# Optimization experiments

Measured on AMD Instinct MI355X. Metric: run time of the kernel, lower is better.

Reference implementation:

```python
import jax, jax.numpy as jnp
import numpy as np

IN_FEATURES = 4096
OUT_FEATURES = 4096
NUM_SUBVECTORS = 32
NUM_CENTROIDS = 256
SUBVECTOR_DIM = IN_FEATURES // NUM_SUBVECTORS
BATCH, SEQ = 4, 2048


def setup_inputs() -> dict:
    key = jax.random.key(0)
    kx, kc, ka = jax.random.split(key, 3)
    x = jax.random.normal(kx, (BATCH, SEQ, IN_FEATURES), dtype=jnp.float32)
    # Stacked per-subvector codebooks: [S, C, d_sub]
    codebooks = jax.random.normal(kc, (NUM_SUBVECTORS, NUM_CENTROIDS, SUBVECTOR_DIM), dtype=jnp.float32)
    assignments = jax.random.randint(ka, (OUT_FEATURES, NUM_SUBVECTORS), 0, NUM_CENTROIDS, dtype=jnp.int32)
    return {"x": x, "codebooks": codebooks, "assignments": assignments}


def reference(x, codebooks, assignments):
    S = codebooks.shape[0]
    # Gather per-subvector centroids: W_parts[o, s, :] = codebooks[s, assignments[o, s], :]
    sub_idx = jnp.arange(S)[None, :]                      # [1, S]
    w_parts = codebooks[sub_idx, assignments]             # [out, S, d_sub]
    W = w_parts.reshape(w_parts.shape[0], -1)             # [out, in] (concat over subvectors)
    return jnp.einsum('bsi,oi->bso', x, W)                # x @ W.T
```

## Files before the change

### kernel.cpp

```cpp
#include <hip/hip_runtime.h>
#include <hip/hip_bf16.h>


#define K_DIM 4096
#define N_DIM 4096
#define M_DIM 8192

typedef __attribute__((ext_vector_type(8))) __bf16 bf16x8;
typedef __attribute__((ext_vector_type(4))) float f32x4;
typedef __attribute__((ext_vector_type(8))) unsigned short ushort8;

__device__ __forceinline__ unsigned short f2bf_rne(float f) {
    unsigned u = __builtin_bit_cast(unsigned, f);
    u += 0x7fffu + ((u >> 16) & 1u);
    return (unsigned short)(u >> 16);
}

__global__ void gather_w_kernel(const float* __restrict__ cb,
                                const int* __restrict__ asn,
                                unsigned short* __restrict__ Wb) {
    for (int gid = blockIdx.x * 256 + threadIdx.x; gid < (N_DIM << 9);
         gid += 2048 * 256) {
        int o = gid >> 9;
        int k = (gid & 511) << 3;
        int s = k >> 7;
        int c = asn[(o << 5) + s];
        const float* src = cb + ((((s << 8) + c) << 7) + (k & 127));
        float4 v0 = *(const float4*)src;
        float4 v1 = *(const float4*)(src + 4);
        ushort8 r;
        r[0] = f2bf_rne(v0.x); r[1] = f2bf_rne(v0.y);
        r[2] = f2bf_rne(v0.z); r[3] = f2bf_rne(v0.w);
        r[4] = f2bf_rne(v1.x); r[5] = f2bf_rne(v1.y);
        r[6] = f2bf_rne(v1.z); r[7] = f2bf_rne(v1.w);
        *(ushort8*)(Wb + (size_t)o * K_DIM + k) = r;
    }
}

__global__ void convert_x_kernel(const float* __restrict__ X,
                                 unsigned short* __restrict__ Xb) {
    for (size_t i = blockIdx.x * 256 + threadIdx.x;
         i < (size_t)M_DIM * K_DIM / 8; i += 2048 * 256) {
        size_t base = i * 8;
        float4 v0 = *(const float4*)(X + base);
        float4 v1 = *(const float4*)(X + base + 4);
        ushort8 r;
        r[0] = f2bf_rne(v0.x); r[1] = f2bf_rne(v0.y);
        r[2] = f2bf_rne(v0.z); r[3] = f2bf_rne(v0.w);
        r[4] = f2bf_rne(v1.x); r[5] = f2bf_rne(v1.y);
        r[6] = f2bf_rne(v1.z); r[7] = f2bf_rne(v1.w);
        *(ushort8*)(Xb + base) = r;
    }
}

#define T_TILES 128
#define SLOT_E  16384

__global__ __launch_bounds__(512, 2) void gemm_pipe_kernel(
    const __bf16* __restrict__ A, const __bf16* __restrict__ B,
    float* __restrict__ C) {
    constexpr int K = K_DIM, N = N_DIM;
    extern __shared__ __bf16 lds[];

    const int tid = threadIdx.x;
    const int w   = tid >> 6;
    const int l   = tid & 63;
    const int wr  = w >> 2;
    const int wc  = w & 3;
    const int lr  = l & 15;
    const int khr = l >> 4;

    const int bid = blockIdx.x;
    const int swz = (bid & 7) * 64 + (bid >> 3);
    const long m0 = (long)(swz >> 4) * 256;
    const long n0 = (long)(swz & 15) * 256;

    const int scol = (((l & 3) ^ ((l >> 3) & 3)) << 3);
    const int srow = w * 32 + (l >> 2);
    const __bf16* gA0 = A + (m0 + srow) * (long)K + scol;
    const __bf16* gA1 = gA0 + 16 * (long)K;
    const __bf16* gB0 = B + (n0 + srow) * (long)K + scol;
    const __bf16* gB1 = gB0 + 16 * (long)K;

    const int sw    = (lr >> 1) & 3;
    const int aoff0 = (wr * 128 + lr) * 32 + ((khr ^ sw) << 3);
    const int boff0 = 8192 + (wc * 64 + lr) * 32 + ((khr ^ sw) << 3);

    f32x4 acc[8][4] = {};

    #define STAGE(t) do {                                                     \
        const int s_ = (t) & 3;                                               \
        __bf16* b_ = lds + s_ * SLOT_E;                                       \
        const int ko_ = (t) * 32;                                             \
        __builtin_amdgcn_global_load_lds(                                     \
            (const __attribute__((address_space(1))) void*)(gA0 + ko_),       \
            (__attribute__((address_space(3))) void*)(b_ + (w * 32) * 32),    \
            16, 0, 0);                                                        \
        __builtin_amdgcn_global_load_lds(                                     \
            (const __attribute__((address_space(1))) void*)(gA1 + ko_),       \
            (__attribute__((address_space(3))) void*)(b_ + (w * 32 + 16) * 32),\
            16, 0, 0);                                                        \
        __builtin_amdgcn_global_load_lds(                                     \
            (const __attribute__((address_space(1))) void*)(gB0 + ko_),       \
            (__attribute__((address_space(3))) void*)(b_ + 8192 + (w * 32) * 32),\
            16, 0, 0);                                                        \
        __builtin_amdgcn_global_load_lds(                                     \
            (const __attribute__((address_space(1))) void*)(gB1 + ko_),       \
            (__attribute__((address_space(3))) void*)(b_ + 8192 + (w * 32 + 16) * 32),\
            16, 0, 0);                                                        \
    } while (0)

    #define COMPUTE(t) do {                                                   \
        const __bf16* pa_ = lds + ((t) & 3) * SLOT_E + aoff0;                 \
        const __bf16* pb_ = lds + ((t) & 3) * SLOT_E + boff0;                 \
        bf16x8 af_[8], bf_[4];                                                \
        _Pragma("unroll")                                                     \
        for (int m = 0; m < 8; ++m) af_[m] = *(const bf16x8*)(pa_ + m * 512); \
        _Pragma("unroll")                                                     \
        for (int n = 0; n < 4; ++n) bf_[n] = *(const bf16x8*)(pb_ + n * 512); \
        __builtin_amdgcn_s_setprio(1);                                        \
        _Pragma("unroll")                                                     \
        for (int m = 0; m < 8; ++m)                                           \
            _Pragma("unroll")                                                 \
            for (int n = 0; n < 4; ++n)                                       \
                acc[m][n] = __builtin_amdgcn_mfma_f32_16x16x32_bf16(          \
                    af_[m], bf_[n], acc[m][n], 0, 0, 0);                      \
        __builtin_amdgcn_s_setprio(0);                                        \
    } while (0)

    STAGE(0); STAGE(1); STAGE(2);

    for (int t = 0; t < T_TILES - 3; ++t) {
        asm volatile("s_waitcnt vmcnt(8)" ::: "memory");
        __builtin_amdgcn_s_barrier();
        STAGE(t + 3);
        COMPUTE(t);
    }
    asm volatile("s_waitcnt vmcnt(8)" ::: "memory");
    __builtin_amdgcn_s_barrier();
    COMPUTE(T_TILES - 3);
    asm volatile("s_waitcnt vmcnt(4)" ::: "memory");
    __builtin_amdgcn_s_barrier();
    COMPUTE(T_TILES - 2);
    asm volatile("s_waitcnt vmcnt(0)" ::: "memory");
    __builtin_amdgcn_s_barrier();
    COMPUTE(T_TILES - 1);

    const int crow = khr * 4;
    #pragma unroll
    for (int m = 0; m < 8; ++m)
        #pragma unroll
        for (int n = 0; n < 4; ++n) {
            float* cp = C + (m0 + wr * 128 + m * 16 + crow) * (long)N
                          + n0 + wc * 64 + n * 16 + lr;
            #pragma unroll
            for (int j = 0; j < 4; ++j) cp[(long)j * N] = acc[m][n][j];
        }
    #undef STAGE
    #undef COMPUTE
}

extern "C" void kernel_launch(void* const* d_in, const int* in_sizes, int n_in,
                              void* d_out, int out_size, void* d_ws, size_t ws_size,
                              hipStream_t stream) {
    const float* x   = (const float*)d_in[0];
    const float* cb  = (const float*)d_in[1];
    const int*   asn = (const int*)d_in[2];
    float* out = (float*)d_out;

    unsigned short* Wb = (unsigned short*)d_ws;
    unsigned short* Xb = Wb + (size_t)N_DIM * K_DIM;

    gather_w_kernel<<<2048, 256, 0, stream>>>(cb, asn, Wb);
    convert_x_kernel<<<2048, 256, 0, stream>>>(x, Xb);
    gemm_pipe_kernel<<<512, 512, 131072, stream>>>(
        (const __bf16*)Xb, (const __bf16*)Wb, out);
}
```

Before: 461.2 us.

## Fuse fp32-to-bf16 conversion of X into the GEMM's A-tile load path

Removes the separate convert_x kernel and the bf16 copy of X. The GEMM now reads fp32 X straight into registers one tile ahead, converts it to bf16 in-kernel and writes a swizzled, double-buffered A tile to LDS, while B keeps its 4-stage direct global-to-LDS pipeline. This saves one full-size read-write pass over X and a kernel launch. In exchange the GEMM reads twice the A bytes from global memory, does conversion ALU work inside the main loop, and uses a more intricate wait-count schedule with an extra lgkmcnt wait per iteration.

After: 653.0 us. +41.6%, slower.

```diff
diff --git a/kernel.cpp b/kernel.cpp
--- a/kernel.cpp
+++ b/kernel.cpp
@@ -37,27 +37,13 @@
     }
 }
 
-__global__ void convert_x_kernel(const float* __restrict__ X,
-                                 unsigned short* __restrict__ Xb) {
-    for (size_t i = blockIdx.x * 256 + threadIdx.x;
-         i < (size_t)M_DIM * K_DIM / 8; i += 2048 * 256) {
-        size_t base = i * 8;
-        float4 v0 = *(const float4*)(X + base);
-        float4 v1 = *(const float4*)(X + base + 4);
-        ushort8 r;
-        r[0] = f2bf_rne(v0.x); r[1] = f2bf_rne(v0.y);
-        r[2] = f2bf_rne(v0.z); r[3] = f2bf_rne(v0.w);
-        r[4] = f2bf_rne(v1.x); r[5] = f2bf_rne(v1.y);
-        r[6] = f2bf_rne(v1.z); r[7] = f2bf_rne(v1.w);
-        *(ushort8*)(Xb + base) = r;
-    }
-}
+#define T_TILES 128
+#define ASLOT_E 8192
+#define BBASE_E 16384
+#define FENCE asm volatile("" ::: "memory")
 
-#define T_TILES 128
-#define SLOT_E  16384
-
-__global__ __launch_bounds__(512, 2) void gemm_pipe_kernel(
-    const __bf16* __restrict__ A, const __bf16* __restrict__ B,
+__global__ __launch_bounds__(512, 2) void gemm_fused_kernel(
+    const float* __restrict__ X, const __bf16* __restrict__ B,
     float* __restrict__ C) {
     constexpr int K = K_DIM, N = N_DIM;
     extern __shared__ __bf16 lds[];
@@ -65,8 +51,7 @@
     const int tid = threadIdx.x;
     const int w   = tid >> 6;
     const int l   = tid & 63;
-    const int wr  = w >> 2;
-    const int wc  = w & 3;
+    const int wr  = w >> 2, wc = w & 3;
     const int lr  = l & 15;
     const int khr = l >> 4;
 
@@ -77,74 +62,97 @@
 
     const int scol = (((l & 3) ^ ((l >> 3) & 3)) << 3);
     const int srow = w * 32 + (l >> 2);
-    const __bf16* gA0 = A + (m0 + srow) * (long)K + scol;
-    const __bf16* gA1 = gA0 + 16 * (long)K;
     const __bf16* gB0 = B + (n0 + srow) * (long)K + scol;
     const __bf16* gB1 = gB0 + 16 * (long)K;
 
+    const int arow = w * 32 + (l >> 1);
+    const float* pX = X + (m0 + arow) * (long)K + ((l & 1) * 16);
+    const int p0 = (2 * (l & 1))     ^ ((l >> 2) & 3);
+    const int p1 = (2 * (l & 1) + 1) ^ ((l >> 2) & 3);
+
     const int sw    = (lr >> 1) & 3;
     const int aoff0 = (wr * 128 + lr) * 32 + ((khr ^ sw) << 3);
-    const int boff0 = 8192 + (wc * 64 + lr) * 32 + ((khr ^ sw) << 3);
+    const int boff0 = (wc * 64 + lr) * 32 + ((khr ^ sw) << 3);
 
     f32x4 acc[8][4] = {};
+    float4 ar0, ar1, ar2, ar3;
 
-    #define STAGE(t) do {                                                     \
-        const int s_ = (t) & 3;                                               \
-        __bf16* b_ = lds + s_ * SLOT_E;                                       \
-        const int ko_ = (t) * 32;                                             \
-        __builtin_amdgcn_global_load_lds(                                     \
-            (const __attribute__((address_space(1))) void*)(gA0 + ko_),       \
-            (__attribute__((address_space(3))) void*)(b_ + (w * 32) * 32),    \
-            16, 0, 0);                                                        \
-        __builtin_amdgcn_global_load_lds(                                     \
-            (const __attribute__((address_space(1))) void*)(gA1 + ko_),       \
-            (__attribute__((address_space(3))) void*)(b_ + (w * 32 + 16) * 32),\
-            16, 0, 0);                                                        \
+    #define A_ISSUE(t) do {                                                   \
+        const float* p_ = pX + (long)(t) * 32;                                \
+        ar0 = *(const float4*)(p_);      ar1 = *(const float4*)(p_ + 4);      \
+        ar2 = *(const float4*)(p_ + 8);  ar3 = *(const float4*)(p_ + 12);     \
+    } while (0)
+
+    #define B_ISSUE(t) do {                                                   \
+        __bf16* bb_ = lds + BBASE_E + ((t) & 3) * ASLOT_E;                    \
+        const long ko_ = (long)(t) * 32;                                      \
         __builtin_amdgcn_global_load_lds(                                     \
             (const __attribute__((address_space(1))) void*)(gB0 + ko_),       \
-            (__attribute__((address_space(3))) void*)(b_ + 8192 + (w * 32) * 32),\
+            (__attribute__((address_space(3))) void*)(bb_ + (w * 32) * 32),   \
             16, 0, 0);                                                        \
         __builtin_amdgcn_global_load_lds(                                     \
             (const __attribute__((address_space(1))) void*)(gB1 + ko_),       \
-            (__attribute__((address_space(3))) void*)(b_ + 8192 + (w * 32 + 16) * 32),\
+            (__attribute__((address_space(3))) void*)(bb_ + (w * 32 + 16) * 32),\
             16, 0, 0);                                                        \
     } while (0)
 
+    #define A_WRITE(t) do {                                                   \
+        __bf16* d_ = lds + ((t) & 1) * ASLOT_E + arow * 32;                   \
+        ushort8 w0, w1;                                                       \
+        w0[0] = f2bf_rne(ar0.x); w0[1] = f2bf_rne(ar0.y);                     \
+        w0[2] = f2bf_rne(ar0.z); w0[3] = f2bf_rne(ar0.w);                     \
+        w0[4] = f2bf_rne(ar1.x); w0[5] = f2bf_rne(ar1.y);                     \
+        w0[6] = f2bf_rne(ar1.z); w0[7] = f2bf_rne(ar1.w);                     \
+        w1[0] = f2bf_rne(ar2.x); w1[1] = f2bf_rne(ar2.y);                     \
+        w1[2] = f2bf_rne(ar2.z); w1[3] = f2bf_rne(ar2.w);                     \
+        w1[4] = f2bf_rne(ar3.x); w1[5] = f2bf_rne(ar3.y);                     \
+        w1[6] = f2bf_rne(ar3.z); w1[7] = f2bf_rne(ar3.w);                     \
+        *(bf16x8*)(d_ + p0 * 8) = __builtin_bit_cast(bf16x8, w0);             \
+        *(bf16x8*)(d_ + p1 * 8) = __builtin_bit_cast(bf16x8, w1);             \
+    } while (0)
+
     #define COMPUTE(t) do {                                                   \
-        const __bf16* pa_ = lds + ((t) & 3) * SLOT_E + aoff0;                 \
-        const __bf16* pb_ = lds + ((t) & 3) * SLOT_E + boff0;                 \
-        bf16x8 af_[8], bf_[4];                                                \
-        _Pragma("unroll")                                                     \
-        for (int m = 0; m < 8; ++m) af_[m] = *(const bf16x8*)(pa_ + m * 512); \
+        const __bf16* pa_ = lds + ((t) & 1) * ASLOT_E + aoff0;                \
+        const __bf16* pb_ = lds + BBASE_E + ((t) & 3) * ASLOT_E + boff0;      \
+        bf16x8 bf_[4];                                                        \
         _Pragma("unroll")                                                     \
         for (int n = 0; n < 4; ++n) bf_[n] = *(const bf16x8*)(pb_ + n * 512); \
         __builtin_amdgcn_s_setprio(1);                                        \
         _Pragma("unroll")                                                     \
-        for (int m = 0; m < 8; ++m)                                           \
+        for (int m = 0; m < 8; ++m) {                                         \
+            bf16x8 af_ = *(const bf16x8*)(pa_ + m * 512);                     \
             _Pragma("unroll")                                                 \
             for (int n = 0; n < 4; ++n)                                       \
                 acc[m][n] = __builtin_amdgcn_mfma_f32_16x16x32_bf16(          \
-                    af_[m], bf_[n], acc[m][n], 0, 0, 0);                      \
+                    af_, bf_[n], acc[m][n], 0, 0, 0);                         \
+        }                                                                     \
         __builtin_amdgcn_s_setprio(0);                                        \
     } while (0)
 
-    STAGE(0); STAGE(1); STAGE(2);
+    #define ITER(t, FS, DA, DB, DW) do {                                      \
+        asm volatile("s_waitcnt vmcnt(" FS ")" ::: "memory");                 \
+        asm volatile("s_waitcnt lgkmcnt(0)" ::: "memory");                    \
+        __builtin_amdgcn_s_barrier();                                         \
+        FENCE;                                                                \
+        if (DA) { A_ISSUE((t) + 1); }                                         \
+        FENCE;                                                                \
+        if (DB) { B_ISSUE((t) + 3); }                                         \
+        FENCE;                                                                \
+        COMPUTE(t);                                                           \
+        if (DW) { A_WRITE((t) + 1); }                                         \
+    } while (0)
 
-    for (int t = 0; t < T_TILES - 3; ++t) {
-        asm volatile("s_waitcnt vmcnt(8)" ::: "memory");
-        __builtin_amdgcn_s_barrier();
-        STAGE(t + 3);
-        COMPUTE(t);
-    }
-    asm volatile("s_waitcnt vmcnt(8)" ::: "memory");
-    __builtin_amdgcn_s_barrier();
-    COMPUTE(T_TILES - 3);
-    asm volatile("s_waitcnt vmcnt(4)" ::: "memory");
-    __builtin_amdgcn_s_barrier();
-    COMPUTE(T_TILES - 2);
-    asm volatile("s_waitcnt vmcnt(0)" ::: "memory");
-    __builtin_amdgcn_s_barrier();
-    COMPUTE(T_TILES - 1);
+    A_ISSUE(0); FENCE;
+    B_ISSUE(0); FENCE; B_ISSUE(1); FENCE; B_ISSUE(2); FENCE;
+    asm volatile("s_waitcnt vmcnt(6)" ::: "memory");
+    A_WRITE(0);
+
+    ITER(0, "4", 1, 1, 1);
+    ITER(1, "8", 1, 1, 1);
+    for (int t = 2; t <= 124; ++t) ITER(t, "12", 1, 1, 1);
+    ITER(125, "12", 1, 0, 1);
+    ITER(126, "10", 1, 0, 1);
+    ITER(127, "8",  0, 0, 0);
 
     const int crow = khr * 4;
     #pragma unroll
@@ -156,8 +164,11 @@
             #pragma unroll
             for (int j = 0; j < 4; ++j) cp[(long)j * N] = acc[m][n][j];
         }
-    #undef STAGE
+    #undef A_ISSUE
+    #undef B_ISSUE
+    #undef A_WRITE
     #undef COMPUTE
+    #undef ITER
 }
 
 extern "C" void kernel_launch(void* const* d_in, const int* in_sizes, int n_in,
@@ -169,10 +180,8 @@
     float* out = (float*)d_out;
 
     unsigned short* Wb = (unsigned short*)d_ws;
-    unsigned short* Xb = Wb + (size_t)N_DIM * K_DIM;
 
     gather_w_kernel<<<2048, 256, 0, stream>>>(cb, asn, Wb);
-    convert_x_kernel<<<2048, 256, 0, stream>>>(x, Xb);
-    gemm_pipe_kernel<<<512, 512, 131072, stream>>>(
-        (const __bf16*)Xb, (const __bf16*)Wb, out);
+    gemm_fused_kernel<<<512, 512, 98304, stream>>>(
+        x, (const __bf16*)Wb, out);
 }
```
